# Kernel optimization log

Hardware: AMD Instinct MI355X
Metric: run time of the kernel (lower is better)

The kernel has to match this reference:

```python
import jax, jax.numpy as jnp
import numpy as np

N_NODES = 50000
N_EDGES = 800000
NF = 64       # input_nf = output_nf = hidden_nf
RADIAL = 1

def tanhshrink(x):
    return x - jnp.tanh(x)

def _linear_params(key, fan_in, fan_out):
    k1, k2 = jax.random.split(key)
    s = 1.0 / np.sqrt(fan_in)
    W = jax.random.uniform(k1, (fan_in, fan_out), jnp.float32, -s, s)
    b = jax.random.uniform(k2, (fan_out,), jnp.float32, -s, s)
    return W, b

def setup_inputs() -> dict:
    key = jax.random.key(0)
    ks = jax.random.split(key, 11)
    nodes = jax.random.normal(ks[0], (N_NODES, NF), jnp.float32)
    coord = jax.random.normal(ks[1], (N_NODES, 3), jnp.float32)
    edges = jax.random.randint(ks[2], (2, N_EDGES), 0, N_NODES, jnp.int64)
    # Edge MLP: Linear(2*NF + RADIAL -> NF), Linear(NF -> NF)
    eW1, eb1 = _linear_params(ks[3], 2 * NF + RADIAL, NF)
    eW2, eb2 = _linear_params(ks[4], NF, NF)
    # Edge attention: Linear(2*NF -> NF), Linear(NF -> 1)
    aW1, ab1 = _linear_params(ks[5], 2 * NF, NF)
    aW2, ab2 = _linear_params(ks[6], NF, 1)
    # Node MLP: Linear(NF + NF -> NF), Linear(NF -> NF)
    nW1, nb1 = _linear_params(ks[7], 2 * NF, NF)
    nW2, nb2 = _linear_params(ks[8], NF, NF)
    # Coord MLP: Linear(NF -> NF), Linear(NF -> 1)
    cW1, cb1 = _linear_params(ks[9], NF, NF)
    cW2, cb2 = _linear_params(ks[10], NF, 1)
    return dict(nodes=nodes, coord=coord, edges=edges,
                eW1=eW1, eb1=eb1, eW2=eW2, eb2=eb2,
                aW1=aW1, ab1=ab1, aW2=aW2, ab2=ab2,
                nW1=nW1, nb1=nb1, nW2=nW2, nb2=nb2,
                cW1=cW1, cb1=cb1, cW2=cW2, cb2=cb2)

def reference(nodes, coord, edges,
              eW1, eb1, eW2, eb2,
              aW1, ab1, aW2, ab2,
              nW1, nb1, nW2, nb2,
              cW1, cb1, cW2, cb2):
    row, col = edges[0], edges[1]
    n = nodes.shape[0]
    # Radial: squared distance along each edge
    rij = coord[row] - coord[col]                       # [E, 3]
    radial = jnp.sum(rij * rij, axis=1, keepdims=True)  # [E, 1]
    src, tgt = nodes[row], nodes[col]                   # [E, NF]
    # Edge MLP with attention gate
    agg_in = jnp.concatenate([src, tgt, radial], axis=1)
    h = tanhshrink(agg_in @ eW1 + eb1)
    h = tanhshrink(h @ eW2 + eb2)                       # [E, NF]
    att_in = jnp.concatenate([src, tgt], axis=1)
    a = tanhshrink(att_in @ aW1 + ab1)
    a = jax.nn.sigmoid(a @ aW2 + ab2)                   # [E, 1]
    edge_feat = h * a                                   # [E, NF]
    # Coordinate update: rij scaled by scalar per edge, scatter-add to row
    c = tanhshrink(edge_feat @ cW1 + cb1)
    trans = rij * (c @ cW2 + cb2)                       # [E, 3]
    coord_out = coord + jax.ops.segment_sum(trans, row, num_segments=n)
    # Node update: scatter-add edge features to row, residual MLP
    agg = jax.ops.segment_sum(edge_feat, row, num_segments=n)  # [N, NF]
    m = jnp.concatenate([nodes, agg], axis=1)
    m = tanhshrink(m @ nW1 + nb1)
    nodes_out = nodes + (m @ nW2 + nb2)
    return nodes_out, coord_out
```

## Files before the change

kernel.cpp:

```cpp
#include <hip/hip_runtime.h>
#include <hip/hip_fp16.h>

#define NF 64

typedef _Float16 half8 __attribute__((ext_vector_type(8)));
typedef float f32x4 __attribute__((ext_vector_type(4)));

__device__ __forceinline__ float ts_f(float x){
  float t = __expf(2.0f*x);
  float th = 1.0f - 2.0f*__builtin_amdgcn_rcpf(t + 1.0f);
  return x - th;
}
__device__ __forceinline__ float sigmoid_f(float x){
  return __builtin_amdgcn_rcpf(1.0f + __expf(-x));
}

__global__ __launch_bounds__(256) void k_prepw_hist(
    const float* __restrict__ eW1, const float* __restrict__ aW1,
    const float* __restrict__ eW2, const float* __restrict__ cW1,
    const float* __restrict__ nW1, const float* __restrict__ nW2,
    _Float16* __restrict__ W256t, _Float16* __restrict__ N1t,
    _Float16* __restrict__ W2t, _Float16* __restrict__ C1t,
    _Float16* __restrict__ N2t,
    const int* __restrict__ edges, int* __restrict__ counts,
    int* __restrict__ rank, int E)
{
  const int bi = blockIdx.x;
  if (bi < 64){
    const int t = bi*256 + threadIdx.x;
    {
      const int n = t >> 6, k = t & 63;
      float v;
      if      (n < 64)  v = eW1[k*NF + n];
      else if (n < 128) v = aW1[k*NF + (n-64)];
      else if (n < 192) v = eW1[(64+k)*NF + (n-128)];
      else              v = aW1[(64+k)*NF + (n-192)];
      W256t[t] = (_Float16)v;
    }
    if (t < 64*128){
      const int n = t >> 7, k = t & 127;
      N1t[t] = (_Float16)nW1[k*NF + n];
    }
    if (t < 64*64){
      const int n = t >> 6, k = t & 63;
      W2t[t] = (_Float16)eW2[k*NF + n];
      C1t[t] = (_Float16)cW1[k*NF + n];
      N2t[t] = (_Float16)nW2[k*NF + n];
    }
  } else {
    const int e = (bi - 64)*256 + threadIdx.x;
    if (e < E) rank[e] = atomicAdd(&counts[edges[e]], 1);
  }
}

__global__ __launch_bounds__(256) void k_scan_zero(
    const int* __restrict__ counts, int* __restrict__ offs,
    int* __restrict__ btot, int* __restrict__ btop, int* __restrict__ done,
    float4* __restrict__ zagg, int naggf4,
    float4* __restrict__ zcoord, int ncoordf4,
    int SCAN_B)
{
  const int t = threadIdx.x;
  const int b = blockIdx.x;
  if (b >= SCAN_B){
    const float4 z = make_float4(0.f,0.f,0.f,0.f);
    const int nthr = (gridDim.x - SCAN_B) * 256;
    const int tid = (b - SCAN_B)*256 + t;
    for (int i = tid; i < naggf4; i += nthr)   zagg[i] = z;
    for (int i = tid; i < ncoordf4; i += nthr) zcoord[i] = z;
    return;
  }

  __shared__ int s[256];
  __shared__ int isLast;
  const int4 c = *(const int4*)(counts + b*1024 + 4*t);
  const int mysum = c.x + c.y + c.z + c.w;
  s[t] = mysum; __syncthreads();
  #pragma unroll
  for (int d=1; d<256; d<<=1){
    const int v = (t>=d) ? s[t-d] : 0; __syncthreads();
    s[t] += v; __syncthreads();
  }
  const int base = (t==0) ? 0 : s[t-1];
  int4 o;
  o.x = base; o.y = base + c.x; o.z = o.y + c.y; o.w = o.z + c.z;
  *(int4*)(offs + b*1024 + 4*t) = o;
  if (t == 255) btot[b] = s[255];

  __threadfence();
  if (t == 0) isLast = (atomicAdd(done, 1) == SCAN_B - 1);
  __syncthreads();
  if (isLast){
    __threadfence();
    const int v = (t < SCAN_B) ? btot[t] : 0;
    s[t] = v; __syncthreads();
    #pragma unroll
    for (int d=1; d<256; d<<=1){
      const int u = (t>=d) ? s[t-d] : 0; __syncthreads();
      s[t] += u; __syncthreads();
    }
    if (t < SCAN_B) btop[t] = (t==0) ? 0 : s[t-1];
  }
}

__global__ __launch_bounds__(64, 8) void k_pre_scatter(
    const float* __restrict__ nodes,
    const float* __restrict__ eb1, const float* __restrict__ ab1,
    const _Float16* __restrict__ W256t,
    _Float16* __restrict__ P, _Float16* __restrict__ Q, int N,
    const int* __restrict__ edges, const int* __restrict__ offs,
    const int* __restrict__ btop, const int* __restrict__ rank,
    int* __restrict__ rs, int* __restrict__ cs, int E,
    int preBlocks)
{
  const int bi = blockIdx.x;
  const int lane = threadIdx.x;
  if (bi >= preBlocks){
    const int e = (bi - preBlocks)*64 + lane;
    if (e < E){
      const int r = edges[e], c = edges[E + e];
      const int pos = btop[r >> 10] + offs[r] + rank[e];
      rs[pos] = r; cs[pos] = c;
    }
    return;
  }

  const int p = lane & 15, q = lane >> 4;
  const int m0 = bi * 16;
  const int row = m0 + p;

  const float* __restrict__ xr = nodes + (size_t)row * NF;
  half8 A[2];
  #pragma unroll
  for (int kt=0; kt<2; kt++){
    const float4 xa = *(const float4*)(xr + kt*32 + q*8);
    const float4 xb = *(const float4*)(xr + kt*32 + q*8 + 4);
    A[kt][0]=(_Float16)xa.x; A[kt][1]=(_Float16)xa.y; A[kt][2]=(_Float16)xa.z; A[kt][3]=(_Float16)xa.w;
    A[kt][4]=(_Float16)xb.x; A[kt][5]=(_Float16)xb.y; A[kt][6]=(_Float16)xb.z; A[kt][7]=(_Float16)xb.w;
  }

  #pragma unroll
  for (int ni=0; ni<16; ni++){
    float b = 0.f;
    if (ni < 4)       b = eb1[16*ni + p];
    else if (ni < 8)  b = ab1[16*(ni-4) + p];
    f32x4 acc = (f32x4){b,b,b,b};
    #pragma unroll
    for (int kt=0; kt<2; kt++){
      const half8 Bf = *(const half8*)(W256t + (size_t)(16*ni + p)*NF + kt*32 + q*8);
      acc = __builtin_amdgcn_mfma_f32_16x16x32_f16(A[kt], Bf, acc, 0,0,0);
    }
    _Float16* __restrict__ dst = (ni < 8 ? P : Q);
    const int colbase = (ni & 7) * 16 + p;
    #pragma unroll
    for (int rr=0; rr<4; rr++)
      dst[(size_t)(m0 + 4*q + rr)*128 + colbase] = (_Float16)acc[rr];
  }
}

__global__ __launch_bounds__(64, 4) void egcl_edge(
    const float* __restrict__ coord,
    const int*   __restrict__ rs, const int* __restrict__ cs,
    const _Float16* __restrict__ P, const _Float16* __restrict__ Q,
    const float* __restrict__ eW1,
    const _Float16* __restrict__ W2t, const float* __restrict__ eb2,
    const float* __restrict__ aW2, const float* __restrict__ ab2,
    const _Float16* __restrict__ C1t, const float* __restrict__ cb1,
    const float* __restrict__ cW2, const float* __restrict__ cb2,
    _Float16* __restrict__ aggh, float* __restrict__ coord_out,
    int E)
{
  __shared__ _Float16 tile[64][72];
  __shared__ float gbuf[64];
  __shared__ float csbuf[64];
  __shared__ float tbuf[64][4];
  __shared__ int   rbuf[64];

  const int lane = threadIdx.x;
  const int p = lane & 15, q = lane >> 4;
  const int e = blockIdx.x * 64 + lane;
  const bool valid = (e < E);
  const int el = valid ? e : (E - 1);

  const int r = rs[el];
  const int c = cs[el];
  rbuf[lane] = valid ? r : -1;

  const float rx = coord[3*r+0] - coord[3*c+0];
  const float ry = coord[3*r+1] - coord[3*c+1];
  const float rz = coord[3*r+2] - coord[3*c+2];
  const float radial = rx*rx + ry*ry + rz*rz;

  const _Float16* __restrict__ Pr = P + (size_t)r * 128;
  const _Float16* __restrict__ Qc = Q + (size_t)c * 128;
  const float* __restrict__ wrad = eW1 + 128*NF;

  half8 Bf[4][2];
  #pragma unroll
  for (int ni=0;ni<4;ni++)
    #pragma unroll
    for (int kt=0;kt<2;kt++)
      Bf[ni][kt] = *(const half8*)(W2t + (size_t)(16*ni + p)*NF + kt*32 + q*8);

  float sp0=0.f, sp1=0.f;
  #pragma unroll
  for (int g=0;g<8;g++){
    const half8 pa = *(const half8*)(Pr + 64 + 8*g);
    const half8 qa = *(const half8*)(Qc + 64 + 8*g);
    #pragma unroll
    for (int j=0;j<8;j++){
      const float v = ts_f((float)pa[j] + (float)qa[j]);
      if (j & 1) sp1 = fmaf(v, aW2[8*g+j], sp1); else sp0 = fmaf(v, aW2[8*g+j], sp0);
    }
  }
  const float gate = sigmoid_f(sp0 + sp1 + ab2[0]);
  gbuf[lane] = gate;

  #pragma unroll
  for (int g=0;g<8;g++){
    const half8 ph = *(const half8*)(Pr + 8*g);
    const half8 qh = *(const half8*)(Qc + 8*g);
    half8 hv;
    #pragma unroll
    for (int j=0;j<8;j++)
      hv[j] = (_Float16)ts_f(fmaf(radial, wrad[8*g+j], (float)ph[j] + (float)qh[j]));
    *(half8*)&tile[lane][8*g] = hv;
  }
  __syncthreads();

  f32x4 acc[4][4];
  #pragma unroll
  for (int ni=0;ni<4;ni++){
    const float b = eb2[16*ni + p];
    #pragma unroll
    for (int mi=0;mi<4;mi++) acc[mi][ni] = (f32x4){b,b,b,b};
  }
  #pragma unroll
  for (int mi=0;mi<4;mi++){
    #pragma unroll
    for (int kt=0;kt<2;kt++){
      const half8 Af = *(const half8*)&tile[16*mi + p][kt*32 + q*8];
      #pragma unroll
      for (int ni=0;ni<4;ni++)
        acc[mi][ni] = __builtin_amdgcn_mfma_f32_16x16x32_f16(Af, Bf[ni][kt], acc[mi][ni], 0,0,0);
    }
  }
  __syncthreads();

  #pragma unroll
  for (int mi=0;mi<4;mi++){
    #pragma unroll
    for (int rr=0;rr<4;rr++){
      const int row = 16*mi + 4*q + rr;
      const float gv = gbuf[row];
      #pragma unroll
      for (int ni=0;ni<4;ni++)
        tile[row][16*ni + p] = (_Float16)(ts_f(acc[mi][ni][rr]) * gv);
    }
  }

  #pragma unroll
  for (int ni=0;ni<4;ni++)
    #pragma unroll
    for (int kt=0;kt<2;kt++)
      Bf[ni][kt] = *(const half8*)(C1t + (size_t)(16*ni + p)*NF + kt*32 + q*8);
  #pragma unroll
  for (int ni=0;ni<4;ni++){
    const float b = cb1[16*ni + p];
    #pragma unroll
    for (int mi=0;mi<4;mi++) acc[mi][ni] = (f32x4){b,b,b,b};
  }
  __syncthreads();
  #pragma unroll
  for (int mi=0;mi<4;mi++){
    #pragma unroll
    for (int kt=0;kt<2;kt++){
      const half8 Af = *(const half8*)&tile[16*mi + p][kt*32 + q*8];
      #pragma unroll
      for (int ni=0;ni<4;ni++)
        acc[mi][ni] = __builtin_amdgcn_mfma_f32_16x16x32_f16(Af, Bf[ni][kt], acc[mi][ni], 0,0,0);
    }
  }

  float part[4][4];
  {
    float w2c[4];
    #pragma unroll
    for (int ni=0;ni<4;ni++) w2c[ni] = cW2[16*ni + p];
    #pragma unroll
    for (int mi=0;mi<4;mi++)
      #pragma unroll
      for (int rr=0;rr<4;rr++){
        float s = 0.f;
        #pragma unroll
        for (int ni=0;ni<4;ni++) s = fmaf(ts_f(acc[mi][ni][rr]), w2c[ni], s);
        part[mi][rr] = s;
      }
  }
  #pragma unroll
  for (int mask=1; mask<16; mask<<=1)
    #pragma unroll
    for (int mi=0;mi<4;mi++)
      #pragma unroll
      for (int rr=0;rr<4;rr++)
        part[mi][rr] += __shfl_xor(part[mi][rr], mask);
  {
    float v = 0.f;
    #pragma unroll
    for (int mi=0;mi<4;mi++)
      #pragma unroll
      for (int rr=0;rr<4;rr++)
        if (((p>>2)==mi) & ((p&3)==rr)) v = part[mi][rr];
    csbuf[16*(p>>2) + 4*q + (p&3)] = v + cb2[0];
  }
  __syncthreads();

  {
    const float cse = csbuf[lane];
    tbuf[lane][0] = rx * cse;
    tbuf[lane][1] = ry * cse;
    tbuf[lane][2] = rz * cse;
  }
  __syncthreads();

  {
    int cur = rbuf[0];
    float runsum = 0.f, rc = 0.f;
    #pragma unroll 1
    for (int eo=0; eo<64; eo++){
      const int rr2 = rbuf[eo];
      if (rr2 != cur){
        const float v0 = __shfl(runsum, 2*lane);
        const float v1 = __shfl(runsum, 2*lane+1);
        if (cur >= 0){
          if (lane < 32){
            __half2 hv; hv.x = __float2half(v0); hv.y = __float2half(v1);
            unsafeAtomicAdd((__half2*)aggh + (size_t)cur*32 + lane, hv);
          }
          if (lane < 3) atomicAdd(coord_out + 3*cur + lane, rc);
        }
        runsum = 0.f; rc = 0.f; cur = rr2;
      }
      runsum += (float)tile[eo][lane];
      if (lane < 3) rc += tbuf[eo][lane];
    }
    const float v0 = __shfl(runsum, 2*lane);
    const float v1 = __shfl(runsum, 2*lane+1);
    if (cur >= 0){
      if (lane < 32){
        __half2 hv; hv.x = __float2half(v0); hv.y = __float2half(v1);
        unsafeAtomicAdd((__half2*)aggh + (size_t)cur*32 + lane, hv);
      }
      if (lane < 3) atomicAdd(coord_out + 3*cur + lane, rc);
    }
  }
}

__global__ __launch_bounds__(64, 8) void egcl_node(
    const float* __restrict__ nodes, const float* __restrict__ coord,
    const _Float16* __restrict__ aggh,
    const _Float16* __restrict__ N1t, const float* __restrict__ nb1,
    const _Float16* __restrict__ N2t, const float* __restrict__ nb2,
    float* __restrict__ out_nodes, float* __restrict__ out_coord, int N)
{
  __shared__ _Float16 t2[16][72];
  const int lane = threadIdx.x;
  const int p = lane & 15, q = lane >> 4;
  const int m0 = blockIdx.x * 16;
  const int row = m0 + p;

  half8 A[4];
  const float* __restrict__ xr = nodes + (size_t)row * NF;
  #pragma unroll
  for (int kt=0; kt<2; kt++){
    const float4 xa = *(const float4*)(xr + kt*32 + q*8);
    const float4 xb = *(const float4*)(xr + kt*32 + q*8 + 4);
    A[kt][0]=(_Float16)xa.x; A[kt][1]=(_Float16)xa.y; A[kt][2]=(_Float16)xa.z; A[kt][3]=(_Float16)xa.w;
    A[kt][4]=(_Float16)xb.x; A[kt][5]=(_Float16)xb.y; A[kt][6]=(_Float16)xb.z; A[kt][7]=(_Float16)xb.w;
  }
  const _Float16* __restrict__ ar = aggh + (size_t)row * NF;
  #pragma unroll
  for (int kt=2; kt<4; kt++)
    A[kt] = *(const half8*)(ar + (kt-2)*32 + q*8);

  f32x4 acc[4];
  #pragma unroll
  for (int ni=0;ni<4;ni++){
    const float b = nb1[16*ni + p];
    acc[ni] = (f32x4){b,b,b,b};
  }
  #pragma unroll
  for (int kt=0; kt<4; kt++){
    #pragma unroll
    for (int ni=0;ni<4;ni++){
      const half8 Bf = *(const half8*)(N1t + (size_t)(16*ni + p)*128 + kt*32 + q*8);
      acc[ni] = __builtin_amdgcn_mfma_f32_16x16x32_f16(A[kt], Bf, acc[ni], 0,0,0);
    }
  }

  #pragma unroll
  for (int ni=0;ni<4;ni++)
    #pragma unroll
    for (int rr=0;rr<4;rr++)
      t2[4*q + rr][16*ni + p] = (_Float16)ts_f(acc[ni][rr]);
  __syncthreads();

  half8 A2[2];
  #pragma unroll
  for (int kt=0; kt<2; kt++)
    A2[kt] = *(const half8*)&t2[p][kt*32 + q*8];

  f32x4 acc2[4];
  #pragma unroll
  for (int ni=0;ni<4;ni++){
    const float b = nb2[16*ni + p];
    acc2[ni] = (f32x4){b,b,b,b};
  }
  #pragma unroll
  for (int kt=0; kt<2; kt++){
    #pragma unroll
    for (int ni=0;ni<4;ni++){
      const half8 Bf = *(const half8*)(N2t + (size_t)(16*ni + p)*NF + kt*32 + q*8);
      acc2[ni] = __builtin_amdgcn_mfma_f32_16x16x32_f16(A2[kt], Bf, acc2[ni], 0,0,0);
    }
  }

  #pragma unroll
  for (int ni=0;ni<4;ni++){
    #pragma unroll
    for (int rr=0;rr<4;rr++){
      const size_t idx = (size_t)(m0 + 4*q + rr)*NF + 16*ni + p;
      out_nodes[idx] = nodes[idx] + acc2[ni][rr];
    }
  }

  if (lane < 48)
    out_coord[(size_t)m0*3 + lane] += coord[(size_t)m0*3 + lane];
}

extern "C" void kernel_launch(void* const* d_in, const int* in_sizes, int n_in,
                              void* d_out, int out_size, void* d_ws, size_t ws_size,
                              hipStream_t stream)
{
  const float* nodes = (const float*)d_in[0];
  const float* coord = (const float*)d_in[1];
  const int*   edges = (const int*)  d_in[2];
  const float* eW1 = (const float*)d_in[3];
  const float* eb1 = (const float*)d_in[4];
  const float* eW2 = (const float*)d_in[5];
  const float* eb2 = (const float*)d_in[6];
  const float* aW1 = (const float*)d_in[7];
  const float* ab1 = (const float*)d_in[8];
  const float* aW2 = (const float*)d_in[9];
  const float* ab2 = (const float*)d_in[10];
  const float* nW1 = (const float*)d_in[11];
  const float* nb1 = (const float*)d_in[12];
  const float* nW2 = (const float*)d_in[13];
  const float* nb2 = (const float*)d_in[14];
  const float* cW1 = (const float*)d_in[15];
  const float* cb1 = (const float*)d_in[16];
  const float* cW2 = (const float*)d_in[17];
  const float* cb2 = (const float*)d_in[18];

  const int E = in_sizes[2] / 2;
  const int N = in_sizes[0] / NF;
  const int SCAN_B = (N + 1023) >> 10;
  const int NBINS  = SCAN_B << 10;
  float* out_nodes = (float*)d_out;
  float* out_coord = out_nodes + (size_t)N * NF;

  char* w = (char*)d_ws;
  _Float16* P     = (_Float16*)w;  w += (size_t)N * 128 * 2;
  _Float16* Qh    = (_Float16*)w;  w += (size_t)N * 128 * 2;
  _Float16* aggh  = (_Float16*)w;  w += (size_t)N * 64 * 2;
  char* zbase = w;
  int* counts     = (int*)w;       w += (size_t)NBINS * 4;
  int* done       = (int*)w;       w += 256;
  const size_t zlen = (size_t)(w - zbase);
  int* offs       = (int*)w;       w += (size_t)NBINS * 4;
  int* btot       = (int*)w;       w += 256*4;
  int* btop       = (int*)w;       w += 256*4;
  int* rank       = (int*)w;       w += (size_t)E * 4;
  int* rs         = (int*)w;       w += (size_t)E * 4;
  int* cs_        = (int*)w;       w += (size_t)E * 4;
  _Float16* W256t = (_Float16*)w;  w += 256*64*2;
  _Float16* N1t   = (_Float16*)w;  w += 64*128*2;
  _Float16* W2t   = (_Float16*)w;  w += 64*64*2;
  _Float16* C1t   = (_Float16*)w;  w += 64*64*2;
  _Float16* N2t   = (_Float16*)w;  w += 64*64*2;

  hipMemsetAsync(zbase, 0, zlen, stream);

  const int histBlocks = (E + 255)/256;
  k_prepw_hist<<<64 + histBlocks, 256, 0, stream>>>(eW1, aW1, eW2, cW1, nW1, nW2,
      W256t, N1t, W2t, C1t, N2t, edges, counts, rank, E);

  const int naggf4   = (int)((size_t)N * 64 * 2 / 16);
  const int ncoordf4 = (N * 3) / 4;
  k_scan_zero<<<SCAN_B + 256, 256, 0, stream>>>(counts, offs, btot, btop, done,
      (float4*)aggh, naggf4, (float4*)out_coord, ncoordf4, SCAN_B);

  const int preBlocks = (N + 15)/16;
  const int scatBlocks = (E + 63)/64;
  k_pre_scatter<<<preBlocks + scatBlocks, 64, 0, stream>>>(nodes, eb1, ab1, W256t,
      P, Qh, N, edges, offs, btop, rank, rs, cs_, E, preBlocks);

  egcl_edge<<<(E + 63)/64, 64, 0, stream>>>(coord, rs, cs_, P, Qh,
      eW1, W2t, eb2, aW2, ab2, C1t, cb1, cW2, cb2,
      aggh, out_coord, E);

  egcl_node<<<(N + 15)/16, 64, 0, stream>>>(nodes, coord, aggh,
      N1t, nb1, N2t, nb2, out_nodes, out_coord, N);
}
```

Measured before the change: 305.5 us.

## Fuse histogram, exclusive scan and zeroing into one kernel via last-block scan

Merges the separate scan/zero kernel into the histogram kernel. The last histogram block to finish, detected with an atomic counter, does the whole exclusive scan over the counts with 256 threads, each summing a sequential chunk. Zeroing of the aggregate and coordinate outputs is moved onto extra blocks of the same launch. This removes one kernel launch and the two-level block-offset lookup in the scatter, at the cost of a serial scan of about 200 elements per thread in a single block at the tail of the kernel.

New measurement: 593.0 us. 94.1% more time.

```diff
diff --git a/kernel.cpp b/kernel.cpp
--- a/kernel.cpp
+++ b/kernel.cpp
@@ -23,11 +23,18 @@
     _Float16* __restrict__ W2t, _Float16* __restrict__ C1t,
     _Float16* __restrict__ N2t,
     const int* __restrict__ edges, int* __restrict__ counts,
-    int* __restrict__ rank, int E)
+    int* __restrict__ rank, int* __restrict__ offs, int* __restrict__ done,
+    float4* __restrict__ zagg, int naggf4,
+    float4* __restrict__ zcoord, int ncoordf4,
+    int E, int N, int histB)
 {
+  __shared__ int s[256];
+  __shared__ int isLast;
   const int bi = blockIdx.x;
+  const int tid = threadIdx.x;
+
   if (bi < 64){
-    const int t = bi*256 + threadIdx.x;
+    const int t = bi*256 + tid;
     {
       const int n = t >> 6, k = t & 63;
       float v;
@@ -47,60 +54,43 @@
       C1t[t] = (_Float16)cW1[k*NF + n];
       N2t[t] = (_Float16)nW2[k*NF + n];
     }
-  } else {
-    const int e = (bi - 64)*256 + threadIdx.x;
-    if (e < E) rank[e] = atomicAdd(&counts[edges[e]], 1);
-  }
-}
-
-__global__ __launch_bounds__(256) void k_scan_zero(
-    const int* __restrict__ counts, int* __restrict__ offs,
-    int* __restrict__ btot, int* __restrict__ btop, int* __restrict__ done,
-    float4* __restrict__ zagg, int naggf4,
-    float4* __restrict__ zcoord, int ncoordf4,
-    int SCAN_B)
-{
-  const int t = threadIdx.x;
-  const int b = blockIdx.x;
-  if (b >= SCAN_B){
+    return;
+  }
+
+  if (bi >= 64 + histB){
+    const int zb = bi - 64 - histB;
+    const int nthr = (gridDim.x - 64 - histB) * 256;
+    const int t0 = zb*256 + tid;
     const float4 z = make_float4(0.f,0.f,0.f,0.f);
-    const int nthr = (gridDim.x - SCAN_B) * 256;
-    const int tid = (b - SCAN_B)*256 + t;
-    for (int i = tid; i < naggf4; i += nthr)   zagg[i] = z;
-    for (int i = tid; i < ncoordf4; i += nthr) zcoord[i] = z;
+    for (int i = t0; i < naggf4; i += nthr)   zagg[i] = z;
+    for (int i = t0; i < ncoordf4; i += nthr) zcoord[i] = z;
     return;
   }
 
-  __shared__ int s[256];
-  __shared__ int isLast;
-  const int4 c = *(const int4*)(counts + b*1024 + 4*t);
-  const int mysum = c.x + c.y + c.z + c.w;
-  s[t] = mysum; __syncthreads();
+  const int e = (bi - 64)*256 + tid;
+  if (e < E) rank[e] = atomicAdd(&counts[edges[e]], 1);
+
+  __threadfence();
+  __syncthreads();
+  if (tid == 0) isLast = (atomicAdd(done, 1) == histB - 1);
+  __syncthreads();
+  if (!isLast) return;
+  __threadfence();
+
+  const int CH = (N + 255) >> 8;
+  const int lo = tid*CH;
+  const int hi = (lo + CH < N) ? lo + CH : N;
+
+  int sum = 0;
+  for (int i = lo; i < hi; i++) sum += counts[i];
+  s[tid] = sum; __syncthreads();
   #pragma unroll
   for (int d=1; d<256; d<<=1){
-    const int v = (t>=d) ? s[t-d] : 0; __syncthreads();
-    s[t] += v; __syncthreads();
-  }
-  const int base = (t==0) ? 0 : s[t-1];
-  int4 o;
-  o.x = base; o.y = base + c.x; o.z = o.y + c.y; o.w = o.z + c.z;
-  *(int4*)(offs + b*1024 + 4*t) = o;
-  if (t == 255) btot[b] = s[255];
-
-  __threadfence();
-  if (t == 0) isLast = (atomicAdd(done, 1) == SCAN_B - 1);
-  __syncthreads();
-  if (isLast){
-    __threadfence();
-    const int v = (t < SCAN_B) ? btot[t] : 0;
-    s[t] = v; __syncthreads();
-    #pragma unroll
-    for (int d=1; d<256; d<<=1){
-      const int u = (t>=d) ? s[t-d] : 0; __syncthreads();
-      s[t] += u; __syncthreads();
-    }
-    if (t < SCAN_B) btop[t] = (t==0) ? 0 : s[t-1];
-  }
+    const int v = (tid>=d) ? s[tid-d] : 0; __syncthreads();
+    s[tid] += v; __syncthreads();
+  }
+  int run = (tid==0) ? 0 : s[tid-1];
+  for (int i = lo; i < hi; i++){ offs[i] = run; run += counts[i]; }
 }
 
 __global__ __launch_bounds__(64, 8) void k_pre_scatter(
@@ -109,7 +99,7 @@
     const _Float16* __restrict__ W256t,
     _Float16* __restrict__ P, _Float16* __restrict__ Q, int N,
     const int* __restrict__ edges, const int* __restrict__ offs,
-    const int* __restrict__ btop, const int* __restrict__ rank,
+    const int* __restrict__ rank,
     int* __restrict__ rs, int* __restrict__ cs, int E,
     int preBlocks)
 {
@@ -119,7 +109,7 @@
     const int e = (bi - preBlocks)*64 + lane;
     if (e < E){
       const int r = edges[e], c = edges[E + e];
-      const int pos = btop[r >> 10] + offs[r] + rank[e];
+      const int pos = offs[r] + rank[e];
       rs[pos] = r; cs[pos] = c;
     }
     return;
@@ -464,8 +454,6 @@
 
   const int E = in_sizes[2] / 2;
   const int N = in_sizes[0] / NF;
-  const int SCAN_B = (N + 1023) >> 10;
-  const int NBINS  = SCAN_B << 10;
   float* out_nodes = (float*)d_out;
   float* out_coord = out_nodes + (size_t)N * NF;
 
@@ -474,12 +462,10 @@
   _Float16* Qh    = (_Float16*)w;  w += (size_t)N * 128 * 2;
   _Float16* aggh  = (_Float16*)w;  w += (size_t)N * 64 * 2;
   char* zbase = w;
-  int* counts     = (int*)w;       w += (size_t)NBINS * 4;
+  int* counts     = (int*)w;       w += (size_t)N * 4;
   int* done       = (int*)w;       w += 256;
   const size_t zlen = (size_t)(w - zbase);
-  int* offs       = (int*)w;       w += (size_t)NBINS * 4;
-  int* btot       = (int*)w;       w += 256*4;
-  int* btop       = (int*)w;       w += 256*4;
+  int* offs       = (int*)w;       w += (size_t)N * 4;
   int* rank       = (int*)w;       w += (size_t)E * 4;
   int* rs         = (int*)w;       w += (size_t)E * 4;
   int* cs_        = (int*)w;       w += (size_t)E * 4;
@@ -491,19 +477,18 @@
 
   hipMemsetAsync(zbase, 0, zlen, stream);
 
-  const int histBlocks = (E + 255)/256;
-  k_prepw_hist<<<64 + histBlocks, 256, 0, stream>>>(eW1, aW1, eW2, cW1, nW1, nW2,
-      W256t, N1t, W2t, C1t, N2t, edges, counts, rank, E);
-
+  const int histB = (E + 255)/256;
   const int naggf4   = (int)((size_t)N * 64 * 2 / 16);
   const int ncoordf4 = (N * 3) / 4;
-  k_scan_zero<<<SCAN_B + 256, 256, 0, stream>>>(counts, offs, btot, btop, done,
-      (float4*)aggh, naggf4, (float4*)out_coord, ncoordf4, SCAN_B);
+  const int zeroB = 1712;
+  k_prepw_hist<<<64 + histB + zeroB, 256, 0, stream>>>(eW1, aW1, eW2, cW1, nW1, nW2,
+      W256t, N1t, W2t, C1t, N2t, edges, counts, rank, offs, done,
+      (float4*)aggh, naggf4, (float4*)out_coord, ncoordf4, E, N, histB);
 
   const int preBlocks = (N + 15)/16;
   const int scatBlocks = (E + 63)/64;
   k_pre_scatter<<<preBlocks + scatBlocks, 64, 0, stream>>>(nodes, eb1, ab1, W256t,
-      P, Qh, N, edges, offs, btop, rank, rs, cs_, E, preBlocks);
+      P, Qh, N, edges, offs, rank, rs, cs_, E, preBlocks);
 
   egcl_edge<<<(E + 63)/64, 64, 0, stream>>>(coord, rs, cs_, P, Qh,
       eW1, W2t, eb2, aW2, ab2, C1t, cb1, cW2, cb2,
```
